# Performance work log

Hardware: AMD Instinct MI355X
Metric: run time of the kernel (lower is better)

The kernel has to match this reference:

```python
import jax, jax.numpy as jnp
import numpy as np

N = 50000
E = 800000
IN, HID, OUT = 128, 128, 64


def setup_inputs() -> dict:
    key = jax.random.key(0)
    ks = jax.random.split(key, 12)
    x = jax.random.normal(ks[0], (N, IN), dtype=jnp.float32)
    src = jax.random.randint(ks[1], (E,), 0, N)
    dst = jax.random.randint(ks[2], (E,), 0, N)
    edge_index = jnp.stack([src, dst]).astype(jnp.int64)
    def lin(k, fan_in, fan_out):
        s = 1.0 / np.sqrt(fan_in)
        return jax.random.uniform(k, (fan_in, fan_out), jnp.float32, -s, s)
    return {
        "x": x,
        "edge_index": edge_index,
        "w_l0": lin(ks[3], IN, HID), "b0": jnp.zeros((HID,), jnp.float32), "w_r0": lin(ks[4], IN, HID),
        "w_l1": lin(ks[5], HID, HID), "b1": jnp.zeros((HID,), jnp.float32), "w_r1": lin(ks[6], HID, HID),
        "w_l2": lin(ks[7], HID, OUT), "b2": jnp.zeros((OUT,), jnp.float32), "w_r2": lin(ks[8], HID, OUT),
    }


def _sage_conv(x, src, dst, w_l, b, w_r, num_nodes):
    # mean aggregation of source features onto destination nodes
    msg = x[src]                                            # [E, d]
    summed = jax.ops.segment_sum(msg, dst, num_segments=num_nodes)  # [N, d]
    deg = jax.ops.segment_sum(jnp.ones((src.shape[0],), x.dtype), dst, num_segments=num_nodes)
    aggr = summed / jnp.maximum(deg, 1.0)[:, None]
    # out = lin_l(aggr) + lin_r(x_root); bias only on lin_l (PyG SAGEConv default)
    return aggr @ w_l + b + x @ w_r


def reference(x, edge_index, w_l0, b0, w_r0, w_l1, b1, w_r1, w_l2, b2, w_r2):
    src, dst = edge_index[0].astype(jnp.int32), edge_index[1].astype(jnp.int32)
    n = x.shape[0]
    h = jax.nn.relu(_sage_conv(x, src, dst, w_l0, b0, w_r0, n))  # dropout: eval mode -> identity
    h = jax.nn.relu(_sage_conv(h, src, dst, w_l1, b1, w_r1, n))
    return _sage_conv(h, src, dst, w_l2, b2, w_r2, n)
```

## Files before the change

### kernel.cpp

```cpp
#include <hip/hip_runtime.h>
#include <cstdint>
#include <cstddef>


#define HID 128
#define NSLICE 8
#define FILL_BLOCKS_PER_SLICE 256
#define FILL_BLOCKS (NSLICE * FILL_BLOCKS_PER_SLICE)
#define GEMM_BLOCKS 1024
#define CAP 64
#define CNT_STRIDE 32

using short8 = __attribute__((ext_vector_type(8))) short;
using f32x4  = __attribute__((ext_vector_type(4))) float;


__device__ __forceinline__ unsigned short f32_to_bf16(float f)
{
    union { float f; unsigned int i; } c; c.f = f;
    const unsigned int x = c.i;
    const unsigned int r = x + 0x7fffu + ((x >> 16) & 1u);
    return (unsigned short)(r >> 16);
}

__device__ __forceinline__ float bf16_hi_to_f32(unsigned int hi16_in_low)
{
    union { unsigned int i; float f; } c; c.i = hi16_in_low << 16;
    return c.f;
}

__device__ __forceinline__ unsigned int pack_bf16(float a, float b)
{
    return ((unsigned int)f32_to_bf16(b) << 16) | (unsigned int)f32_to_bf16(a);
}


#define PREP_THREADS (2 * 2 * HID * HID + 2 * 64 * HID)

__global__ __launch_bounds__(256) void prep_wt_zero_kernel(
    const float* __restrict__ wl0, const float* __restrict__ wr0,
    const float* __restrict__ wl1, const float* __restrict__ wr1,
    const float* __restrict__ wl2, const float* __restrict__ wr2,
    unsigned short* __restrict__ wt0, unsigned short* __restrict__ wt1,
    unsigned short* __restrict__ wt2, int* __restrict__ cnt, int n)
{
    const int idx = blockIdx.x * 256 + threadIdx.x;
    const int per128 = 2 * HID * HID;
    if (idx < per128) {
        const int k = idx & (HID - 1), c = idx >> 7;
        const float v = (c < HID) ? wl0[(size_t)k * HID + c] : wr0[(size_t)k * HID + (c - HID)];
        wt0[idx] = f32_to_bf16(v);
    } else if (idx < 2 * per128) {
        const int j = idx - per128;
        const int k = j & (HID - 1), c = j >> 7;
        const float v = (c < HID) ? wl1[(size_t)k * HID + c] : wr1[(size_t)k * HID + (c - HID)];
        wt1[j] = f32_to_bf16(v);
    } else if (idx < PREP_THREADS) {
        const int j = idx - 2 * per128;
        const int k = j & (HID - 1), c = j >> 7;
        const float v = (c < 64) ? wl2[(size_t)k * 64 + c] : wr2[(size_t)k * 64 + (c - 64)];
        wt2[j] = f32_to_bf16(v);
    } else {
        const int j = idx - PREP_THREADS;
        if (j < n) cnt[(size_t)j * CNT_STRIDE] = 0;
    }
}


__device__ __forceinline__ void fill_body(
    int bid, const int* __restrict__ src, const int* __restrict__ dst,
    int* __restrict__ cnt, int* __restrict__ esrc, int E, int n)
{
    const int slice = bid & (NSLICE - 1);
    const int nps   = (n + NSLICE - 1) / NSLICE;
    const int lo    = slice * nps;
    const int hi    = min(lo + nps, n);
    const int stride = FILL_BLOCKS_PER_SLICE * 256;
    int e = (bid >> 3) * 256 + threadIdx.x;
    for (; e < E; e += stride) {
        const int d = dst[e];
        if (d >= lo && d < hi) {
            const int s = src[e];
            if ((unsigned)s < (unsigned)n) {
                const int p = atomicAdd(&cnt[(size_t)d * CNT_STRIDE], 1);
                if (p < CAP) esrc[(size_t)d * CAP + p] = s;
            }
        }
    }
}


template <int DOUT, bool IN_F32, bool R_BF16>
__device__ __forceinline__ void gemm_body(
    int bid, int nblk,
    const void* __restrict__ hin, const unsigned short* __restrict__ wtc,
    const float* __restrict__ bias,
    unsigned short* __restrict__ p, void* __restrict__ r, int n)
{
    constexpr int CPW = (2 * DOUT) / 64;

    const int tx   = threadIdx.x;
    const int wv   = tx >> 6;
    const int lane = tx & 63;
    const int quad = lane >> 4;
    const int l15  = lane & 15;

    short8 B[CPW][4];
#pragma unroll
    for (int t = 0; t < CPW; ++t) {
        const int c = (wv * CPW + t) * 16 + l15;
#pragma unroll
        for (int q = 0; q < 4; ++q)
            B[t][q] = *(const short8*)(wtc + (size_t)c * HID + q * 32 + quad * 8);
    }

    const int slabs = (n + 15) >> 4;
    for (int slab = bid; slab < slabs; slab += nblk) {
        const int r0 = slab * 16;
        const int rr = min(r0 + l15, n - 1);

        short8 A[4];
        if (IN_F32) {
            const float* hf = (const float*)hin;
#pragma unroll
            for (int q = 0; q < 4; ++q) {
                const float4 f0 = *(const float4*)(hf + (size_t)rr * HID + q * 32 + quad * 8);
                const float4 f1 = *(const float4*)(hf + (size_t)rr * HID + q * 32 + quad * 8 + 4);
                short8 a;
                a[0] = (short)f32_to_bf16(f0.x); a[1] = (short)f32_to_bf16(f0.y);
                a[2] = (short)f32_to_bf16(f0.z); a[3] = (short)f32_to_bf16(f0.w);
                a[4] = (short)f32_to_bf16(f1.x); a[5] = (short)f32_to_bf16(f1.y);
                a[6] = (short)f32_to_bf16(f1.z); a[7] = (short)f32_to_bf16(f1.w);
                A[q] = a;
            }
        } else {
            const unsigned short* hb = (const unsigned short*)hin;
#pragma unroll
            for (int q = 0; q < 4; ++q)
                A[q] = *(const short8*)(hb + (size_t)rr * HID + q * 32 + quad * 8);
        }

        f32x4 acc[CPW];
#pragma unroll
        for (int t = 0; t < CPW; ++t) acc[t] = (f32x4){0.f, 0.f, 0.f, 0.f};
#pragma unroll
        for (int q = 0; q < 4; ++q)
#pragma unroll
            for (int t = 0; t < CPW; ++t)
                acc[t] = __builtin_amdgcn_mfma_f32_16x16x32_bf16(A[q], B[t][q], acc[t], 0, 0, 0);

#pragma unroll
        for (int t = 0; t < CPW; ++t) {
            const int c0  = (wv * CPW + t) * 16;
            const int col = c0 + l15;
            if (c0 < DOUT) {
#pragma unroll
                for (int i = 0; i < 4; ++i) {
                    const int row = r0 + quad * 4 + i;
                    if (row < n) p[(size_t)row * DOUT + col] = f32_to_bf16(acc[t][i]);
                }
            } else {
                const float bv = bias[col - DOUT];
#pragma unroll
                for (int i = 0; i < 4; ++i) {
                    const int row = r0 + quad * 4 + i;
                    if (row < n) {
                        const float v = acc[t][i] + bv;
                        if (R_BF16)
                            ((unsigned short*)r)[(size_t)row * DOUT + (col - DOUT)] = f32_to_bf16(v);
                        else
                            ((float*)r)[(size_t)row * DOUT + (col - DOUT)] = v;
                    }
                }
            }
        }
    }
}

template <int DOUT, bool IN_F32, bool R_BF16>
__global__ __launch_bounds__(256) void sage_mfma_gemm(
    const void* __restrict__ hin, const unsigned short* __restrict__ wtc,
    const float* __restrict__ bias,
    unsigned short* __restrict__ p, void* __restrict__ r, int n)
{
    gemm_body<DOUT, IN_F32, R_BF16>(blockIdx.x, gridDim.x, hin, wtc, bias, p, r, n);
}


__global__ __launch_bounds__(256) void fill_gemm0_fused_kernel(
    const int* __restrict__ src, const int* __restrict__ dst,
    int* __restrict__ cnt, int* __restrict__ esrc, int E,
    const void* __restrict__ x, const unsigned short* __restrict__ wt0,
    const float* __restrict__ b0,
    unsigned short* __restrict__ p, void* __restrict__ r, int n)
{
    if (blockIdx.x < FILL_BLOCKS)
        fill_body(blockIdx.x, src, dst, cnt, esrc, E, n);
    else
        gemm_body<128, true, true>(blockIdx.x - FILL_BLOCKS, GEMM_BLOCKS, x, wt0, b0, p, r, n);
}


template <int DOUT, bool RELU, bool OUTBF16, bool R_BF16>
__global__ __launch_bounds__(256) void sage_post_aggregate(
    const unsigned short* __restrict__ p, const void* __restrict__ r,
    const int* __restrict__ cnt, const int* __restrict__ esrc,
    void* __restrict__ out, int n)
{
    const int wid  = threadIdx.x >> 6;
    const int lane = threadIdx.x & 63;
    const int node = blockIdx.x * 4 + wid;
    if (node >= n) return;
    const int dg   = cnt[(size_t)node * CNT_STRIDE];
    const int degc = min(dg, CAP);
    const float inv = 1.0f / fmaxf((float)dg, 1.0f);

    const int sidx = esrc[(size_t)node * CAP + lane];

    if constexpr (DOUT == 128) {
        const int g  = lane >> 4;
        const int lo = lane & 15;
        float acc[4][8];
#pragma unroll
        for (int j = 0; j < 4; ++j)
#pragma unroll
            for (int c = 0; c < 8; ++c) acc[j][c] = 0.f;

        for (int e0 = 0; e0 < degc; e0 += 16) {
#pragma unroll
            for (int j = 0; j < 4; ++j) {
                const int slot = e0 + j * 4 + g;
                const float w  = (slot < degc) ? 1.0f : 0.0f;
                const int s    = __shfl(sidx, min(slot, degc - 1), 64);
                const short8 v = *(const short8*)(p + (size_t)s * DOUT + lo * 8);
#pragma unroll
                for (int c = 0; c < 8; ++c)
                    acc[j][c] = fmaf(w, bf16_hi_to_f32((unsigned short)v[c]), acc[j][c]);
            }
        }
        float s8[8];
#pragma unroll
        for (int c = 0; c < 8; ++c) {
            float t = (acc[0][c] + acc[1][c]) + (acc[2][c] + acc[3][c]);
            t += __shfl_xor(t, 16, 64);
            t += __shfl_xor(t, 32, 64);
            s8[c] = t * inv;
        }
        if (g == 0) {
            float rc[8];
            if (R_BF16) {
                const short8 rv = *(const short8*)((const unsigned short*)r + (size_t)node * DOUT + lo * 8);
#pragma unroll
                for (int c = 0; c < 8; ++c) rc[c] = bf16_hi_to_f32((unsigned short)rv[c]);
            } else {
                const float4 r0 = *(const float4*)((const float*)r + (size_t)node * DOUT + lo * 8);
                const float4 r1 = *(const float4*)((const float*)r + (size_t)node * DOUT + lo * 8 + 4);
                rc[0] = r0.x; rc[1] = r0.y; rc[2] = r0.z; rc[3] = r0.w;
                rc[4] = r1.x; rc[5] = r1.y; rc[6] = r1.z; rc[7] = r1.w;
            }
            float o[8];
#pragma unroll
            for (int c = 0; c < 8; ++c) {
                o[c] = s8[c] + rc[c];
                if (RELU) o[c] = fmaxf(o[c], 0.f);
            }
            if (OUTBF16) {
                uint4 st;
                st.x = pack_bf16(o[0], o[1]); st.y = pack_bf16(o[2], o[3]);
                st.z = pack_bf16(o[4], o[5]); st.w = pack_bf16(o[6], o[7]);
                *(uint4*)((unsigned short*)out + (size_t)node * DOUT + lo * 8) = st;
            } else {
                float4 s0, s1;
                s0.x = o[0]; s0.y = o[1]; s0.z = o[2]; s0.w = o[3];
                s1.x = o[4]; s1.y = o[5]; s1.z = o[6]; s1.w = o[7];
                *(float4*)((float*)out + (size_t)node * DOUT + lo * 8) = s0;
                *(float4*)((float*)out + (size_t)node * DOUT + lo * 8 + 4) = s1;
            }
        }
    } else {
        const int g  = lane >> 3;
        const int lo = lane & 7;
        float acc[2][8];
#pragma unroll
        for (int j = 0; j < 2; ++j)
#pragma unroll
            for (int c = 0; c < 8; ++c) acc[j][c] = 0.f;

        for (int e0 = 0; e0 < degc; e0 += 16) {
#pragma unroll
            for (int j = 0; j < 2; ++j) {
                const int slot = e0 + j * 8 + g;
                const float w  = (slot < degc) ? 1.0f : 0.0f;
                const int s    = __shfl(sidx, min(slot, degc - 1), 64);
                const short8 v = *(const short8*)(p + (size_t)s * DOUT + lo * 8);
#pragma unroll
                for (int c = 0; c < 8; ++c)
                    acc[j][c] = fmaf(w, bf16_hi_to_f32((unsigned short)v[c]), acc[j][c]);
            }
        }
        float s8[8];
#pragma unroll
        for (int c = 0; c < 8; ++c) {
            float t = acc[0][c] + acc[1][c];
            t += __shfl_xor(t, 8, 64);
            t += __shfl_xor(t, 16, 64);
            t += __shfl_xor(t, 32, 64);
            s8[c] = t * inv;
        }
        if (g == 0) {
            float rc[8];
            if (R_BF16) {
                const short8 rv = *(const short8*)((const unsigned short*)r + (size_t)node * DOUT + lo * 8);
#pragma unroll
                for (int c = 0; c < 8; ++c) rc[c] = bf16_hi_to_f32((unsigned short)rv[c]);
            } else {
                const float4 r0 = *(const float4*)((const float*)r + (size_t)node * DOUT + lo * 8);
                const float4 r1 = *(const float4*)((const float*)r + (size_t)node * DOUT + lo * 8 + 4);
                rc[0] = r0.x; rc[1] = r0.y; rc[2] = r0.z; rc[3] = r0.w;
                rc[4] = r1.x; rc[5] = r1.y; rc[6] = r1.z; rc[7] = r1.w;
            }
            float o[8];
#pragma unroll
            for (int c = 0; c < 8; ++c) {
                o[c] = s8[c] + rc[c];
                if (RELU) o[c] = fmaxf(o[c], 0.f);
            }
            if (OUTBF16) {
                uint4 st;
                st.x = pack_bf16(o[0], o[1]); st.y = pack_bf16(o[2], o[3]);
                st.z = pack_bf16(o[4], o[5]); st.w = pack_bf16(o[6], o[7]);
                *(uint4*)((unsigned short*)out + (size_t)node * DOUT + lo * 8) = st;
            } else {
                float4 s0, s1;
                s0.x = o[0]; s0.y = o[1]; s0.z = o[2]; s0.w = o[3];
                s1.x = o[4]; s1.y = o[5]; s1.z = o[6]; s1.w = o[7];
                *(float4*)((float*)out + (size_t)node * DOUT + lo * 8) = s0;
                *(float4*)((float*)out + (size_t)node * DOUT + lo * 8 + 4) = s1;
            }
        }
    }
}


static inline size_t align_up(size_t v, size_t a) { return (v + a - 1) & ~(a - 1); }

extern "C" void kernel_launch(void* const* d_in, const int* in_sizes, int n_in,
                              void* d_out, int out_size, void* d_ws, size_t ws_size,
                              hipStream_t stream)
{
    const float* x   = (const float*)d_in[0];
    const int*   ei  = (const int*)d_in[1];
    const float* wl0 = (const float*)d_in[2];
    const float* b0  = (const float*)d_in[3];
    const float* wr0 = (const float*)d_in[4];
    const float* wl1 = (const float*)d_in[5];
    const float* b1  = (const float*)d_in[6];
    const float* wr1 = (const float*)d_in[7];
    const float* wl2 = (const float*)d_in[8];
    const float* b2  = (const float*)d_in[9];
    const float* wr2 = (const float*)d_in[10];
    float*       out = (float*)d_out;

    const int N = in_sizes[0] / HID;
    const int E = in_sizes[1] / 2;
    const int* src = ei;
    const int* dst = ei + E;

    char*  ws  = (char*)d_ws;
    size_t off = 0;
    int* cnt      = (int*)(ws + off); off = align_up(off + (size_t)N * CNT_STRIDE * 4, 256);
    int* esrc     = (int*)(ws + off); off = align_up(off + (size_t)N * CAP * 4, 256);
    unsigned short* pbuf = (unsigned short*)(ws + off); off = align_up(off + (size_t)N * HID * 2, 256);
    unsigned short* rb16 = (unsigned short*)(ws + off); off = align_up(off + (size_t)N * HID * 2, 256);
    float* rbf32  = (float*)(ws + off); off = align_up(off + (size_t)N * HID * 4, 256);
    unsigned short* hbf = (unsigned short*)(ws + off); off = align_up(off + (size_t)N * HID * 2, 256);
    unsigned short* wt0 = (unsigned short*)(ws + off); off = align_up(off + (size_t)2 * HID * HID * 2, 256);
    unsigned short* wt1 = (unsigned short*)(ws + off); off = align_up(off + (size_t)2 * HID * HID * 2, 256);
    unsigned short* wt2 = (unsigned short*)(ws + off); off = align_up(off + (size_t)HID * HID * 2, 256);
    (void)ws_size; (void)n_in; (void)out_size;

    prep_wt_zero_kernel<<<(PREP_THREADS + N + 255) / 256, 256, 0, stream>>>(
        wl0, wr0, wl1, wr1, wl2, wr2, wt0, wt1, wt2, cnt, N);

    const int aggGrid = (N + 3) / 4;

    fill_gemm0_fused_kernel<<<FILL_BLOCKS + GEMM_BLOCKS, 256, 0, stream>>>(
        src, dst, cnt, esrc, E, x, wt0, b0, pbuf, rb16, N);

    sage_post_aggregate<128, true, true, true><<<aggGrid, 256, 0, stream>>>(pbuf, rb16, cnt, esrc, hbf, N);

    sage_mfma_gemm<128, false, true><<<GEMM_BLOCKS, 256, 0, stream>>>(hbf, wt1, b1, pbuf, rb16, N);
    sage_post_aggregate<128, true, true, true><<<aggGrid, 256, 0, stream>>>(pbuf, rb16, cnt, esrc, hbf, N);

    sage_mfma_gemm<64, false, false><<<GEMM_BLOCKS, 256, 0, stream>>>(hbf, wt2, b2, pbuf, rbf32, N);
    sage_post_aggregate<64, false, false, false><<<aggGrid, 256, 0, stream>>>(pbuf, rbf32, cnt, esrc, out, N);
}
```

Measured before the change: 300.1 us.

## Bucket edge lists by source range and split fill from layer-0 GEMM

The per-destination edge list is split into 8 sub-buckets keyed by source-id range, each with its own counter and a 16-slot capacity. The aggregation kernel reconstructs a source-sorted order by prefix-summing the sub-counts, so neighbour gathers come out roughly sorted by source, which may improve locality. The fill is also moved out of the fused fill+GEMM kernel into its own launch, giving up the overlap between the two. The per-bucket cap of 16 can drop edges that the previous single cap of 64 kept, and the aggregation prologue does more shuffles.

Measured after the change: 300.6 us. Within noise of the previous version (+0.2%).

```diff
diff --git a/kernel.cpp b/kernel.cpp
--- a/kernel.cpp
+++ b/kernel.cpp
@@ -8,7 +8,9 @@
 #define FILL_BLOCKS_PER_SLICE 256
 #define FILL_BLOCKS (NSLICE * FILL_BLOCKS_PER_SLICE)
 #define GEMM_BLOCKS 1024
-#define CAP 64
+#define NSB 8
+#define CAP_SUB 16
+#define ROW_INTS (NSB * CAP_SUB)
 #define CNT_STRIDE 32
 
 using short8 = __attribute__((ext_vector_type(8))) short;
@@ -62,28 +64,29 @@
         wt2[j] = f32_to_bf16(v);
     } else {
         const int j = idx - PREP_THREADS;
-        if (j < n) cnt[(size_t)j * CNT_STRIDE] = 0;
+        if (j < n * NSB) cnt[(size_t)(j >> 3) * CNT_STRIDE + (j & 7)] = 0;
     }
 }
 
 
-__device__ __forceinline__ void fill_body(
-    int bid, const int* __restrict__ src, const int* __restrict__ dst,
-    int* __restrict__ cnt, int* __restrict__ esrc, int E, int n)
-{
-    const int slice = bid & (NSLICE - 1);
+__global__ __launch_bounds__(256) void bucket_fill_sliced_kernel(
+    const int* __restrict__ src, const int* __restrict__ dst,
+    int* __restrict__ cnt, int* __restrict__ esrc, int E, int n, float invN8)
+{
+    const int slice = blockIdx.x & (NSLICE - 1);
     const int nps   = (n + NSLICE - 1) / NSLICE;
     const int lo    = slice * nps;
     const int hi    = min(lo + nps, n);
     const int stride = FILL_BLOCKS_PER_SLICE * 256;
-    int e = (bid >> 3) * 256 + threadIdx.x;
+    int e = (blockIdx.x >> 3) * 256 + threadIdx.x;
     for (; e < E; e += stride) {
         const int d = dst[e];
         if (d >= lo && d < hi) {
             const int s = src[e];
             if ((unsigned)s < (unsigned)n) {
-                const int p = atomicAdd(&cnt[(size_t)d * CNT_STRIDE], 1);
-                if (p < CAP) esrc[(size_t)d * CAP + p] = s;
+                const int sb = min(NSB - 1, (int)((float)s * invN8));
+                const int p  = atomicAdd(&cnt[(size_t)d * CNT_STRIDE + sb], 1);
+                if (p < CAP_SUB) esrc[(size_t)d * ROW_INTS + sb * CAP_SUB + p] = s;
             }
         }
     }
@@ -91,9 +94,9 @@
 
 
 template <int DOUT, bool IN_F32, bool R_BF16>
-__device__ __forceinline__ void gemm_body(
-    int bid, int nblk,
-    const void* __restrict__ hin, const unsigned short* __restrict__ wtc,
+__global__ __launch_bounds__(256) void sage_mfma_gemm(
+    const void* __restrict__ hin,
+    const unsigned short* __restrict__ wtc,
     const float* __restrict__ bias,
     unsigned short* __restrict__ p, void* __restrict__ r, int n)
 {
@@ -115,7 +118,7 @@
     }
 
     const int slabs = (n + 15) >> 4;
-    for (int slab = bid; slab < slabs; slab += nblk) {
+    for (int slab = blockIdx.x; slab < slabs; slab += gridDim.x) {
         const int r0 = slab * 16;
         const int rr = min(r0 + l15, n - 1);
 
@@ -177,29 +180,6 @@
     }
 }
 
-template <int DOUT, bool IN_F32, bool R_BF16>
-__global__ __launch_bounds__(256) void sage_mfma_gemm(
-    const void* __restrict__ hin, const unsigned short* __restrict__ wtc,
-    const float* __restrict__ bias,
-    unsigned short* __restrict__ p, void* __restrict__ r, int n)
-{
-    gemm_body<DOUT, IN_F32, R_BF16>(blockIdx.x, gridDim.x, hin, wtc, bias, p, r, n);
-}
-
-
-__global__ __launch_bounds__(256) void fill_gemm0_fused_kernel(
-    const int* __restrict__ src, const int* __restrict__ dst,
-    int* __restrict__ cnt, int* __restrict__ esrc, int E,
-    const void* __restrict__ x, const unsigned short* __restrict__ wt0,
-    const float* __restrict__ b0,
-    unsigned short* __restrict__ p, void* __restrict__ r, int n)
-{
-    if (blockIdx.x < FILL_BLOCKS)
-        fill_body(blockIdx.x, src, dst, cnt, esrc, E, n);
-    else
-        gemm_body<128, true, true>(blockIdx.x - FILL_BLOCKS, GEMM_BLOCKS, x, wt0, b0, p, r, n);
-}
-
 
 template <int DOUT, bool RELU, bool OUTBF16, bool R_BF16>
 __global__ __launch_bounds__(256) void sage_post_aggregate(
@@ -211,11 +191,34 @@
     const int lane = threadIdx.x & 63;
     const int node = blockIdx.x * 4 + wid;
     if (node >= n) return;
-    const int dg   = cnt[(size_t)node * CNT_STRIDE];
-    const int degc = min(dg, CAP);
+
+    const int craw = cnt[(size_t)node * CNT_STRIDE + (lane & 7)];
+    const int ccap = min(craw, CAP_SUB);
+    const int c0 = __shfl(ccap, 0, 64), c1 = __shfl(ccap, 1, 64);
+    const int c2 = __shfl(ccap, 2, 64), c3 = __shfl(ccap, 3, 64);
+    const int c4 = __shfl(ccap, 4, 64), c5 = __shfl(ccap, 5, 64);
+    const int c6 = __shfl(ccap, 6, 64), c7 = __shfl(ccap, 7, 64);
+    const int r0_ = __shfl(craw, 0, 64), r1_ = __shfl(craw, 1, 64);
+    const int r2_ = __shfl(craw, 2, 64), r3_ = __shfl(craw, 3, 64);
+    const int r4_ = __shfl(craw, 4, 64), r5_ = __shfl(craw, 5, 64);
+    const int r6_ = __shfl(craw, 6, 64), r7_ = __shfl(craw, 7, 64);
+    const int dg = ((r0_ + r1_) + (r2_ + r3_)) + ((r4_ + r5_) + (r6_ + r7_));
+    const int C1 = c0, C2 = C1 + c1, C3 = C2 + c2, C4 = C3 + c3;
+    const int C5 = C4 + c4, C6 = C5 + c5, C7 = C6 + c6;
+    const int T  = C7 + c7;
+    const int degc = min(T, 64);
     const float inv = 1.0f / fmaxf((float)dg, 1.0f);
 
-    const int sidx = esrc[(size_t)node * CAP + lane];
+    const int t = min(lane, max(degc - 1, 0));
+    int sb = 0, off = 0;
+    if (t >= C1) { sb = 1; off = C1; }
+    if (t >= C2) { sb = 2; off = C2; }
+    if (t >= C3) { sb = 3; off = C3; }
+    if (t >= C4) { sb = 4; off = C4; }
+    if (t >= C5) { sb = 5; off = C5; }
+    if (t >= C6) { sb = 6; off = C6; }
+    if (t >= C7) { sb = 7; off = C7; }
+    const int sidx = esrc[(size_t)node * ROW_INTS + sb * CAP_SUB + (t - off)];
 
     if constexpr (DOUT == 128) {
         const int g  = lane >> 4;
@@ -241,10 +244,10 @@
         float s8[8];
 #pragma unroll
         for (int c = 0; c < 8; ++c) {
-            float t = (acc[0][c] + acc[1][c]) + (acc[2][c] + acc[3][c]);
-            t += __shfl_xor(t, 16, 64);
-            t += __shfl_xor(t, 32, 64);
-            s8[c] = t * inv;
+            float t2 = (acc[0][c] + acc[1][c]) + (acc[2][c] + acc[3][c]);
+            t2 += __shfl_xor(t2, 16, 64);
+            t2 += __shfl_xor(t2, 32, 64);
+            s8[c] = t2 * inv;
         }
         if (g == 0) {
             float rc[8];
@@ -253,10 +256,10 @@
 #pragma unroll
                 for (int c = 0; c < 8; ++c) rc[c] = bf16_hi_to_f32((unsigned short)rv[c]);
             } else {
-                const float4 r0 = *(const float4*)((const float*)r + (size_t)node * DOUT + lo * 8);
-                const float4 r1 = *(const float4*)((const float*)r + (size_t)node * DOUT + lo * 8 + 4);
-                rc[0] = r0.x; rc[1] = r0.y; rc[2] = r0.z; rc[3] = r0.w;
-                rc[4] = r1.x; rc[5] = r1.y; rc[6] = r1.z; rc[7] = r1.w;
+                const float4 q0 = *(const float4*)((const float*)r + (size_t)node * DOUT + lo * 8);
+                const float4 q1 = *(const float4*)((const float*)r + (size_t)node * DOUT + lo * 8 + 4);
+                rc[0] = q0.x; rc[1] = q0.y; rc[2] = q0.z; rc[3] = q0.w;
+                rc[4] = q1.x; rc[5] = q1.y; rc[6] = q1.z; rc[7] = q1.w;
             }
             float o[8];
 #pragma unroll
@@ -301,11 +304,11 @@
         float s8[8];
 #pragma unroll
         for (int c = 0; c < 8; ++c) {
-            float t = acc[0][c] + acc[1][c];
-            t += __shfl_xor(t, 8, 64);
-            t += __shfl_xor(t, 16, 64);
-            t += __shfl_xor(t, 32, 64);
-            s8[c] = t * inv;
+            float t2 = acc[0][c] + acc[1][c];
+            t2 += __shfl_xor(t2, 8, 64);
+            t2 += __shfl_xor(t2, 16, 64);
+            t2 += __shfl_xor(t2, 32, 64);
+            s8[c] = t2 * inv;
         }
         if (g == 0) {
             float rc[8];
@@ -314,10 +317,10 @@
 #pragma unroll
                 for (int c = 0; c < 8; ++c) rc[c] = bf16_hi_to_f32((unsigned short)rv[c]);
             } else {
-                const float4 r0 = *(const float4*)((const float*)r + (size_t)node * DOUT + lo * 8);
-                const float4 r1 = *(const float4*)((const float*)r + (size_t)node * DOUT + lo * 8 + 4);
-                rc[0] = r0.x; rc[1] = r0.y; rc[2] = r0.z; rc[3] = r0.w;
-                rc[4] = r1.x; rc[5] = r1.y; rc[6] = r1.z; rc[7] = r1.w;
+                const float4 q0 = *(const float4*)((const float*)r + (size_t)node * DOUT + lo * 8);
+                const float4 q1 = *(const float4*)((const float*)r + (size_t)node * DOUT + lo * 8 + 4);
+                rc[0] = q0.x; rc[1] = q0.y; rc[2] = q0.z; rc[3] = q0.w;
+                rc[4] = q1.x; rc[5] = q1.y; rc[6] = q1.z; rc[7] = q1.w;
             }
             float o[8];
 #pragma unroll
@@ -369,7 +372,7 @@
     char*  ws  = (char*)d_ws;
     size_t off = 0;
     int* cnt      = (int*)(ws + off); off = align_up(off + (size_t)N * CNT_STRIDE * 4, 256);
-    int* esrc     = (int*)(ws + off); off = align_up(off + (size_t)N * CAP * 4, 256);
+    int* esrc     = (int*)(ws + off); off = align_up(off + (size_t)N * ROW_INTS * 4, 256);
     unsigned short* pbuf = (unsigned short*)(ws + off); off = align_up(off + (size_t)N * HID * 2, 256);
     unsigned short* rb16 = (unsigned short*)(ws + off); off = align_up(off + (size_t)N * HID * 2, 256);
     float* rbf32  = (float*)(ws + off); off = align_up(off + (size_t)N * HID * 4, 256);
@@ -379,14 +382,16 @@
     unsigned short* wt2 = (unsigned short*)(ws + off); off = align_up(off + (size_t)HID * HID * 2, 256);
     (void)ws_size; (void)n_in; (void)out_size;
 
-    prep_wt_zero_kernel<<<(PREP_THREADS + N + 255) / 256, 256, 0, stream>>>(
+    prep_wt_zero_kernel<<<(PREP_THREADS + NSB * N + 255) / 256, 256, 0, stream>>>(
         wl0, wr0, wl1, wr1, wl2, wr2, wt0, wt1, wt2, cnt, N);
 
+    const float invN8 = (float)NSB / (float)N;
+    bucket_fill_sliced_kernel<<<FILL_BLOCKS, 256, 0, stream>>>(
+        src, dst, cnt, esrc, E, N, invN8);
+
     const int aggGrid = (N + 3) / 4;
 
-    fill_gemm0_fused_kernel<<<FILL_BLOCKS + GEMM_BLOCKS, 256, 0, stream>>>(
-        src, dst, cnt, esrc, E, x, wt0, b0, pbuf, rb16, N);
-
+    sage_mfma_gemm<128, true, true><<<GEMM_BLOCKS, 256, 0, stream>>>(x, wt0, b0, pbuf, rb16, N);
     sage_post_aggregate<128, true, true, true><<<aggGrid, 256, 0, stream>>>(pbuf, rb16, cnt, esrc, hbf, N);
 
     sage_mfma_gemm<128, false, true><<<GEMM_BLOCKS, 256, 0, stream>>>(hbf, wt1, b1, pbuf, rb16, N);
```
